# Optimization experiments

Hardware: AMD Instinct MI355X
Metric: run time of the kernel (lower is better)

The kernel has to match this reference:

```python
import jax, jax.numpy as jnp
import numpy as np

N_CAMS = 2000
N_PTS = 500000
N_OBS = 5000000


def quat_rotate(q, v):
    """Rotate vectors v [..., 3] by quaternions q [..., 4] in (x, y, z, w) order (pypose convention)."""
    qv, qw = q[..., :3], q[..., 3:4]
    uv = jnp.cross(qv, v)
    uuv = jnp.cross(qv, uv)
    return v + 2.0 * (qw * uv + uuv)


def setup_inputs() -> dict:
    key = jax.random.key(0)
    k0, k1, k2, k3, k4, k5, k6 = jax.random.split(key, 7)
    observe = jax.random.normal(k0, (N_OBS, 2), dtype=jnp.float32)
    cidx = jax.random.randint(k1, (N_OBS,), 0, N_CAMS)
    pidx = jax.random.randint(k2, (N_OBS,), 0, N_PTS)
    # Camera intrinsics: (focal, k1, k2)
    K = jnp.concatenate([
        500.0 + 10.0 * jax.random.normal(k3, (N_CAMS, 1), dtype=jnp.float32),
        0.01 * jax.random.normal(k3, (N_CAMS, 2), dtype=jnp.float32),
    ], axis=-1)
    # SE3 poses (tx,ty,tz,qx,qy,qz,qw): near-identity rotation, z-offset translation
    t = 0.1 * jax.random.normal(k4, (N_CAMS, 3), dtype=jnp.float32)
    t = t.at[:, 2].add(10.0)  # keep points in front of cameras (cp_z ~ 10)
    qv = 0.05 * jax.random.normal(k5, (N_CAMS, 3), dtype=jnp.float32)
    q = jnp.concatenate([qv, jnp.ones((N_CAMS, 1), dtype=jnp.float32)], axis=-1)
    q = q / jnp.linalg.norm(q, axis=-1, keepdims=True)
    C = jnp.concatenate([t, q], axis=-1)
    P = jax.random.normal(k6, (N_PTS, 3), dtype=jnp.float32)
    return {"observe": observe, "cidx": cidx, "pidx": pidx, "K": K, "C": C, "P": P}


def reference(observe, cidx, pidx, K, C, P):
    Kc = K[cidx]          # [N_OBS, 3]
    Cc = C[cidx]          # [N_OBS, 7]
    Pp = P[pidx]          # [N_OBS, 3]
    t, q = Cc[:, :3], Cc[:, 3:7]
    cp = quat_rotate(q, Pp) + t                    # SE3 action
    n = -cp[:, :2] / cp[:, 2:3]                    # perspective divide
    radius = jnp.sum(n * n, axis=-1, keepdims=True)
    focal, k1, k2 = Kc[:, :1], Kc[:, 1:2], Kc[:, 2:3]
    distortion = 1.0 + k1 * radius + k2 * radius * radius
    return focal * distortion * n - observe
```

## Files before the change

kernel.cpp:

```cpp
#include <hip/hip_runtime.h>


typedef int      vi4 __attribute__((ext_vector_type(4)));
typedef float    vf4 __attribute__((ext_vector_type(4)));
typedef float    vf2 __attribute__((ext_vector_type(2)));
typedef float    vf3 __attribute__((ext_vector_type(3), aligned(4)));
typedef _Float16 vh4 __attribute__((ext_vector_type(4)));

__global__ __launch_bounds__(1024) void cvt_p_kernel(
    const float* __restrict__ P, vh4* __restrict__ P16, int npts)
{
    int i4 = (blockIdx.x * 1024 + threadIdx.x) * 4;
    if (i4 + 4 <= npts) {
        vf4 a = *(const vf4*)(P + 3 * i4);
        vf4 b = *(const vf4*)(P + 3 * i4 + 4);
        vf4 c = *(const vf4*)(P + 3 * i4 + 8);
        vh4 h0 = { (_Float16)a.x, (_Float16)a.y, (_Float16)a.z, (_Float16)0.f };
        vh4 h1 = { (_Float16)a.w, (_Float16)b.x, (_Float16)b.y, (_Float16)0.f };
        vh4 h2 = { (_Float16)b.z, (_Float16)b.w, (_Float16)c.x, (_Float16)0.f };
        vh4 h3 = { (_Float16)c.y, (_Float16)c.z, (_Float16)c.w, (_Float16)0.f };
        P16[i4 + 0] = h0; P16[i4 + 1] = h1; P16[i4 + 2] = h2; P16[i4 + 3] = h3;
    } else {
        for (int i = i4; i < npts; ++i) {
            vh4 h = { (_Float16)P[3 * i], (_Float16)P[3 * i + 1],
                      (_Float16)P[3 * i + 2], (_Float16)0.f };
            P16[i] = h;
        }
    }
}

__device__ __forceinline__ void reproj_one(
    float vx, float vy, float vz,
    vf4 q, vf4 tf, vf2 d,
    float obx, float oby, float* ox, float* oy)
{
    float qx = q.x, qy = q.y, qz = q.z, qw = q.w;
    float tx = tf.x, ty = tf.y, tz = tf.z, f = tf.w;
    float k1 = d.x, k2 = d.y;

    float uvx = qy * vz - qz * vy;
    float uvy = qz * vx - qx * vz;
    float uvz = qx * vy - qy * vx;
    float uuvx = qy * uvz - qz * uvy;
    float uuvy = qz * uvx - qx * uvz;
    float uuvz = qx * uvy - qy * uvx;

    float cpx = vx + 2.0f * (qw * uvx + uuvx) + tx;
    float cpy = vy + 2.0f * (qw * uvy + uuvy) + ty;
    float cpz = vz + 2.0f * (qw * uvz + uuvz) + tz;

    float inv = 1.0f / cpz;
    float nx = -cpx * inv;
    float ny = -cpy * inv;
    float r  = nx * nx + ny * ny;

    float dist = 1.0f + k1 * r + k2 * r * r;
    float fd   = f * dist;

    *ox = fd * nx - obx;
    *oy = fd * ny - oby;
}

__global__ __launch_bounds__(1024, 4) void reproj_kernel(
    const float*  __restrict__ observe,
    const int*    __restrict__ cidx,
    const int*    __restrict__ pidx,
    const float*  __restrict__ K,
    const float*  __restrict__ C,
    const vh4*    __restrict__ P16,
    float*        __restrict__ out,
    int n, int ncams)
{
    extern __shared__ float lds[];
    vf4* Qs = (vf4*)lds;
    vf4* Ts = (vf4*)(lds + 4 * ncams);
    vf2* Ds = (vf2*)(lds + 8 * ncams);

    for (int c = threadIdx.x; c < ncams; c += 1024) {
        const float* Cc = C + 7 * c;
        const float* Kc = K + 3 * c;
        vf4 q  = { Cc[3], Cc[4], Cc[5], Cc[6] };
        vf4 tf = { Cc[0], Cc[1], Cc[2], Kc[0] };
        vf2 d  = { Kc[1], Kc[2] };
        Qs[c] = q; Ts[c] = tf; Ds[c] = d;
    }
    __syncthreads();

    const int stride = gridDim.x * 1024 * 4;
    int base = (blockIdx.x * 1024 + threadIdx.x) * 4;
    if (base >= n) return;
    if (base + 4 > n) {
        for (int i = base; i < n; ++i) {
            int c = cidx[i];
            vh4 h = P16[pidx[i]];
            float ox, oy;
            reproj_one((float)h.x, (float)h.y, (float)h.z, Qs[c], Ts[c], Ds[c],
                       observe[2 * i], observe[2 * i + 1], &ox, &oy);
            out[2 * i] = ox; out[2 * i + 1] = oy;
        }
        return;
    }

    vi4 cA = __builtin_nontemporal_load((const vi4*)(cidx + base));
    vi4 pA = __builtin_nontemporal_load((const vi4*)(pidx + base));
    vf4 obA0 = __builtin_nontemporal_load((const vf4*)(observe + 2 * base));
    vf4 obA1 = __builtin_nontemporal_load((const vf4*)(observe + 2 * base + 4));
    vh4 hA0 = P16[pA.x];
    vh4 hA1 = P16[pA.y];
    vh4 hA2 = P16[pA.z];
    vh4 hA3 = P16[pA.w];

    for (;;) {
        int next = base + stride;
        bool have_next = (next + 4 <= n);

        vi4 cB, pB; vf4 obB0, obB1;
        if (have_next) {
            cB   = __builtin_nontemporal_load((const vi4*)(cidx + next));
            pB   = __builtin_nontemporal_load((const vi4*)(pidx + next));
            obB0 = __builtin_nontemporal_load((const vf4*)(observe + 2 * next));
            obB1 = __builtin_nontemporal_load((const vf4*)(observe + 2 * next + 4));
        }

        float r0, r1, r2, r3, r4, r5, r6, r7;
        reproj_one((float)hA0.x, (float)hA0.y, (float)hA0.z,
                   Qs[cA.x], Ts[cA.x], Ds[cA.x], obA0.x, obA0.y, &r0, &r1);
        reproj_one((float)hA1.x, (float)hA1.y, (float)hA1.z,
                   Qs[cA.y], Ts[cA.y], Ds[cA.y], obA0.z, obA0.w, &r2, &r3);
        reproj_one((float)hA2.x, (float)hA2.y, (float)hA2.z,
                   Qs[cA.z], Ts[cA.z], Ds[cA.z], obA1.x, obA1.y, &r4, &r5);
        reproj_one((float)hA3.x, (float)hA3.y, (float)hA3.z,
                   Qs[cA.w], Ts[cA.w], Ds[cA.w], obA1.z, obA1.w, &r6, &r7);

        vf4 o0 = { r0, r1, r2, r3 };
        vf4 o1 = { r4, r5, r6, r7 };
        __builtin_nontemporal_store(o0, (vf4*)(out + 2 * base));
        __builtin_nontemporal_store(o1, (vf4*)(out + 2 * base + 4));

        if (!have_next) break;

        cA = cB; obA0 = obB0; obA1 = obB1;
        hA0 = P16[pB.x];
        hA1 = P16[pB.y];
        hA2 = P16[pB.z];
        hA3 = P16[pB.w];
        base = next;
    }
}

extern "C" void kernel_launch(void* const* d_in, const int* in_sizes, int n_in,
                              void* d_out, int out_size, void* d_ws, size_t ws_size,
                              hipStream_t stream)
{
    const float* observe = (const float*)d_in[0];
    const int*   cidx    = (const int*)d_in[1];
    const int*   pidx    = (const int*)d_in[2];
    const float* K       = (const float*)d_in[3];
    const float* C       = (const float*)d_in[4];
    const float* P       = (const float*)d_in[5];
    float*       out     = (float*)d_out;

    int n     = in_sizes[1];
    int ncams = in_sizes[3] / 3;
    int npts  = in_sizes[5] / 3;

    vh4* P16 = (vh4*)d_ws;

    int cthreads = (npts + 3) / 4;
    int cgrid = (cthreads + 1023) / 1024;
    cvt_p_kernel<<<cgrid, 1024, 0, stream>>>(P, P16, npts);

    int block = 1024;
    int grid  = 256;
    int need  = (n + block * 4 - 1) / (block * 4);
    if (grid > need) grid = need;
    size_t lds_bytes = (size_t)ncams * 10 * sizeof(float);

    reproj_kernel<<<grid, block, lds_bytes, stream>>>(
        observe, cidx, pidx, K, C, P16, out, n, ncams);
}
```

Before: 61.49 us.

## Fuse point fp16 conversion into main kernel with grid-wide barrier

Removes the separate P-to-fp16 conversion kernel. Each block now converts a slice of P at the start of the main kernel, then all blocks wait on an atomic grid-wide barrier before the gather phase, and a memset resets the barrier counter. An fp32 fallback path is used when the workspace is too small to hold the fp16 copy and the counter. The divide is also replaced by a hardware reciprocal. The aim is to save a kernel launch and its tail, at the cost of an extra memset, a spin barrier that only works if all 256 blocks are resident at once, and slightly lower accuracy in the reciprocal.

```diff
diff --git a/kernel.cpp b/kernel.cpp
--- a/kernel.cpp
+++ b/kernel.cpp
@@ -6,28 +6,6 @@
 typedef float    vf2 __attribute__((ext_vector_type(2)));
 typedef float    vf3 __attribute__((ext_vector_type(3), aligned(4)));
 typedef _Float16 vh4 __attribute__((ext_vector_type(4)));
-
-__global__ __launch_bounds__(1024) void cvt_p_kernel(
-    const float* __restrict__ P, vh4* __restrict__ P16, int npts)
-{
-    int i4 = (blockIdx.x * 1024 + threadIdx.x) * 4;
-    if (i4 + 4 <= npts) {
-        vf4 a = *(const vf4*)(P + 3 * i4);
-        vf4 b = *(const vf4*)(P + 3 * i4 + 4);
-        vf4 c = *(const vf4*)(P + 3 * i4 + 8);
-        vh4 h0 = { (_Float16)a.x, (_Float16)a.y, (_Float16)a.z, (_Float16)0.f };
-        vh4 h1 = { (_Float16)a.w, (_Float16)b.x, (_Float16)b.y, (_Float16)0.f };
-        vh4 h2 = { (_Float16)b.z, (_Float16)b.w, (_Float16)c.x, (_Float16)0.f };
-        vh4 h3 = { (_Float16)c.y, (_Float16)c.z, (_Float16)c.w, (_Float16)0.f };
-        P16[i4 + 0] = h0; P16[i4 + 1] = h1; P16[i4 + 2] = h2; P16[i4 + 3] = h3;
-    } else {
-        for (int i = i4; i < npts; ++i) {
-            vh4 h = { (_Float16)P[3 * i], (_Float16)P[3 * i + 1],
-                      (_Float16)P[3 * i + 2], (_Float16)0.f };
-            P16[i] = h;
-        }
-    }
-}
 
 __device__ __forceinline__ void reproj_one(
     float vx, float vy, float vz,
@@ -49,7 +27,7 @@
     float cpy = vy + 2.0f * (qw * uvy + uuvy) + ty;
     float cpz = vz + 2.0f * (qw * uvz + uuvz) + tz;
 
-    float inv = 1.0f / cpz;
+    float inv = __builtin_amdgcn_rcpf(cpz);
     float nx = -cpx * inv;
     float ny = -cpy * inv;
     float r  = nx * nx + ny * ny;
@@ -61,20 +39,50 @@
     *oy = fd * ny - oby;
 }
 
-__global__ __launch_bounds__(1024, 4) void reproj_kernel(
+template <bool H>
+__device__ __forceinline__ vf3 load_pt(const vh4* __restrict__ P16,
+                                       const float* __restrict__ P, int i)
+{
+    if (H) {
+        vh4 h = P16[i];
+        vf3 r = { (float)h.x, (float)h.y, (float)h.z };
+        return r;
+    } else {
+        return *(const vf3*)(P + 3 * i);
+    }
+}
+
+template <bool USE_HALF>
+__global__ __launch_bounds__(1024, 4) void fused_kernel(
     const float*  __restrict__ observe,
     const int*    __restrict__ cidx,
     const int*    __restrict__ pidx,
     const float*  __restrict__ K,
     const float*  __restrict__ C,
-    const vh4*    __restrict__ P16,
+    const float*  __restrict__ P,
+    vh4*          __restrict__ P16,
+    unsigned int* __restrict__ bar,
     float*        __restrict__ out,
-    int n, int ncams)
+    int n, int ncams, int npts)
 {
     extern __shared__ float lds[];
     vf4* Qs = (vf4*)lds;
     vf4* Ts = (vf4*)(lds + 4 * ncams);
     vf2* Ds = (vf2*)(lds + 8 * ncams);
+
+    if (USE_HALF) {
+        int nb  = (int)gridDim.x;
+        int ppb = (npts + nb - 1) / nb;
+        int lo  = blockIdx.x * ppb;
+        int hi  = lo + ppb; if (hi > npts) hi = npts;
+        for (int i = lo + (int)threadIdx.x; i < hi; i += 1024) {
+            vf3 v = *(const vf3*)(P + 3 * i);
+            vh4 h = { (_Float16)v.x, (_Float16)v.y, (_Float16)v.z, (_Float16)0.f };
+            unsigned long long bits = __builtin_bit_cast(unsigned long long, h);
+            __hip_atomic_store((unsigned long long*)(P16 + i), bits,
+                               __ATOMIC_RELAXED, __HIP_MEMORY_SCOPE_AGENT);
+        }
+    }
 
     for (int c = threadIdx.x; c < ncams; c += 1024) {
         const float* Cc = C + 7 * c;
@@ -86,15 +94,29 @@
     }
     __syncthreads();
 
+    if (USE_HALF) {
+        if (threadIdx.x == 0) {
+            __threadfence();
+            __hip_atomic_fetch_add(bar, 1u, __ATOMIC_ACQ_REL,
+                                   __HIP_MEMORY_SCOPE_AGENT);
+            unsigned int nb = gridDim.x;
+            while (__hip_atomic_load(bar, __ATOMIC_ACQUIRE,
+                                     __HIP_MEMORY_SCOPE_AGENT) < nb)
+                __builtin_amdgcn_s_sleep(2);
+            __threadfence();
+        }
+        __syncthreads();
+    }
+
     const int stride = gridDim.x * 1024 * 4;
     int base = (blockIdx.x * 1024 + threadIdx.x) * 4;
     if (base >= n) return;
     if (base + 4 > n) {
         for (int i = base; i < n; ++i) {
             int c = cidx[i];
-            vh4 h = P16[pidx[i]];
+            vf3 pv = load_pt<USE_HALF>(P16, P, pidx[i]);
             float ox, oy;
-            reproj_one((float)h.x, (float)h.y, (float)h.z, Qs[c], Ts[c], Ds[c],
+            reproj_one(pv.x, pv.y, pv.z, Qs[c], Ts[c], Ds[c],
                        observe[2 * i], observe[2 * i + 1], &ox, &oy);
             out[2 * i] = ox; out[2 * i + 1] = oy;
         }
@@ -105,10 +127,10 @@
     vi4 pA = __builtin_nontemporal_load((const vi4*)(pidx + base));
     vf4 obA0 = __builtin_nontemporal_load((const vf4*)(observe + 2 * base));
     vf4 obA1 = __builtin_nontemporal_load((const vf4*)(observe + 2 * base + 4));
-    vh4 hA0 = P16[pA.x];
-    vh4 hA1 = P16[pA.y];
-    vh4 hA2 = P16[pA.z];
-    vh4 hA3 = P16[pA.w];
+    vf3 hA0 = load_pt<USE_HALF>(P16, P, pA.x);
+    vf3 hA1 = load_pt<USE_HALF>(P16, P, pA.y);
+    vf3 hA2 = load_pt<USE_HALF>(P16, P, pA.z);
+    vf3 hA3 = load_pt<USE_HALF>(P16, P, pA.w);
 
     for (;;) {
         int next = base + stride;
@@ -123,14 +145,14 @@
         }
 
         float r0, r1, r2, r3, r4, r5, r6, r7;
-        reproj_one((float)hA0.x, (float)hA0.y, (float)hA0.z,
-                   Qs[cA.x], Ts[cA.x], Ds[cA.x], obA0.x, obA0.y, &r0, &r1);
-        reproj_one((float)hA1.x, (float)hA1.y, (float)hA1.z,
-                   Qs[cA.y], Ts[cA.y], Ds[cA.y], obA0.z, obA0.w, &r2, &r3);
-        reproj_one((float)hA2.x, (float)hA2.y, (float)hA2.z,
-                   Qs[cA.z], Ts[cA.z], Ds[cA.z], obA1.x, obA1.y, &r4, &r5);
-        reproj_one((float)hA3.x, (float)hA3.y, (float)hA3.z,
-                   Qs[cA.w], Ts[cA.w], Ds[cA.w], obA1.z, obA1.w, &r6, &r7);
+        reproj_one(hA0.x, hA0.y, hA0.z, Qs[cA.x], Ts[cA.x], Ds[cA.x],
+                   obA0.x, obA0.y, &r0, &r1);
+        reproj_one(hA1.x, hA1.y, hA1.z, Qs[cA.y], Ts[cA.y], Ds[cA.y],
+                   obA0.z, obA0.w, &r2, &r3);
+        reproj_one(hA2.x, hA2.y, hA2.z, Qs[cA.z], Ts[cA.z], Ds[cA.z],
+                   obA1.x, obA1.y, &r4, &r5);
+        reproj_one(hA3.x, hA3.y, hA3.z, Qs[cA.w], Ts[cA.w], Ds[cA.w],
+                   obA1.z, obA1.w, &r6, &r7);
 
         vf4 o0 = { r0, r1, r2, r3 };
         vf4 o1 = { r4, r5, r6, r7 };
@@ -140,10 +162,10 @@
         if (!have_next) break;
 
         cA = cB; obA0 = obB0; obA1 = obB1;
-        hA0 = P16[pB.x];
-        hA1 = P16[pB.y];
-        hA2 = P16[pB.z];
-        hA3 = P16[pB.w];
+        hA0 = load_pt<USE_HALF>(P16, P, pB.x);
+        hA1 = load_pt<USE_HALF>(P16, P, pB.y);
+        hA2 = load_pt<USE_HALF>(P16, P, pB.z);
+        hA3 = load_pt<USE_HALF>(P16, P, pB.w);
         base = next;
     }
 }
@@ -164,11 +186,12 @@
     int ncams = in_sizes[3] / 3;
     int npts  = in_sizes[5] / 3;
 
-    vh4* P16 = (vh4*)d_ws;
-
-    int cthreads = (npts + 3) / 4;
-    int cgrid = (cthreads + 1023) / 1024;
-    cvt_p_kernel<<<cgrid, 1024, 0, stream>>>(P, P16, npts);
+    size_t p16_bytes = (size_t)npts * 8;
+    size_t bar_off   = (p16_bytes + 255) & ~(size_t)255;
+    bool use_half    = (ws_size >= bar_off + 256);
+
+    vh4*          P16 = (vh4*)d_ws;
+    unsigned int* bar = (unsigned int*)((char*)d_ws + bar_off);
 
     int block = 1024;
     int grid  = 256;
@@ -176,6 +199,12 @@
     if (grid > need) grid = need;
     size_t lds_bytes = (size_t)ncams * 10 * sizeof(float);
 
-    reproj_kernel<<<grid, block, lds_bytes, stream>>>(
-        observe, cidx, pidx, K, C, P16, out, n, ncams);
-}
+    if (use_half) {
+        hipMemsetAsync(bar, 0, sizeof(unsigned int), stream);
+        fused_kernel<true><<<grid, block, lds_bytes, stream>>>(
+            observe, cidx, pidx, K, C, P, P16, bar, out, n, ncams, npts);
+    } else {
+        fused_kernel<false><<<grid, block, lds_bytes, stream>>>(
+            observe, cidx, pidx, K, C, P, P16, bar, out, n, ncams, npts);
+    }
+}
```

Result: slower. 92.82 us (+50.9%).
